# Optimization experiments

Measured on AMD Instinct MI355X. Metric: run time of the kernel, lower is better.

The kernel has to match this reference:

```python
import jax, jax.numpy as jnp
import numpy as np

N = 100_000        # nodes
E = 3_200_000      # edges (avg degree 32)
F_IN = 256         # feature_num
HID = 32           # hard-coded hidden dim in TwoLayerModel
F_OUT = 64         # output_num


def setup_inputs() -> dict:
    key = jax.random.key(0)
    k0, k1, k2, k3 = jax.random.split(key, 4)
    x = jax.random.normal(k0, (N, F_IN), dtype=jnp.float32)
    edge_index = jax.random.randint(k1, (2, E), 0, N, dtype=jnp.int32)
    # glorot-ish init for the two linear weights, zero bias (matches reset_parameters)
    W1 = jax.random.normal(k2, (F_IN, HID), dtype=jnp.float32) * np.float32(1.0 / np.sqrt(F_IN))
    b1 = jnp.zeros((HID,), dtype=jnp.float32)
    W2 = jax.random.normal(k3, (HID, F_OUT), dtype=jnp.float32) * np.float32(1.0 / np.sqrt(HID))
    b2 = jnp.zeros((F_OUT,), dtype=jnp.float32)
    return {"x": x, "edge_index": edge_index, "W1": W1, "b1": b1, "W2": W2, "b2": b2}


def _gcn_propagate(h, row, col, n):
    """Symmetric-normalized sum aggregation: out[i] = sum_{(j->i)} d_j^-1/2 d_i^-1/2 h[j].
    Matches PyG gcn_norm / NewSampleModelLayer edge_weight (deg computed on col)."""
    deg = jax.ops.segment_sum(jnp.ones_like(col, dtype=h.dtype), col, num_segments=n)
    dinv = jnp.where(deg > 0, deg ** -0.5, 0.0)
    norm = dinv[row] * dinv[col]                      # [E']
    return jax.ops.segment_sum(norm[:, None] * h[row], col, num_segments=n)


def reference(x, edge_index, W1, b1, W2, b2):
    n = x.shape[0]
    sl = jnp.arange(n, dtype=edge_index.dtype)
    row = jnp.concatenate([edge_index[0], sl])        # add self-loops
    col = jnp.concatenate([edge_index[1], sl])
    # layer 1: GCNConv(feature_num, 32) -> relu (dropout inactive in eval)
    h = _gcn_propagate(x @ W1, row, col, n) + b1
    h = jax.nn.relu(h)
    # layer 2 (NewSampleModelLayer, eval path): propagate then linear projection
    fr = _gcn_propagate(h, row, col, n)
    return fr @ W2 + b2
```

## Files before the change

### kernel.cpp

```cpp
#include <hip/hip_runtime.h>
#include <hip/hip_fp16.h>
#include <math.h>


#define SHIFT1 8
#define S1 256
#define MAXNB1 400

typedef _Float16 half8 __attribute__((ext_vector_type(8)));
typedef float f32x4 __attribute__((ext_vector_type(4)));

__global__ void k_zero(int* p, int n) {
    int i = blockIdx.x * blockDim.x + threadIdx.x;
    if (i < n) p[i] = 0;
}

__global__ void k_hist1(const int4* __restrict__ cols4, int* __restrict__ bcnt,
                        int e4, int etail, const int* __restrict__ cols, int nb) {
    __shared__ int h[MAXNB1];
    for (int i = threadIdx.x; i < nb; i += blockDim.x) h[i] = 0;
    __syncthreads();
    for (int i = blockIdx.x * blockDim.x + threadIdx.x; i < e4; i += gridDim.x * blockDim.x) {
        int4 c = cols4[i];
        atomicAdd(&h[c.x >> SHIFT1], 1);
        atomicAdd(&h[c.y >> SHIFT1], 1);
        atomicAdd(&h[c.z >> SHIFT1], 1);
        atomicAdd(&h[c.w >> SHIFT1], 1);
    }
    if (blockIdx.x == 0 && threadIdx.x < etail)
        atomicAdd(&h[cols[e4 * 4 + threadIdx.x] >> SHIFT1], 1);
    __syncthreads();
    for (int i = threadIdx.x; i < nb; i += blockDim.x)
        if (h[i]) atomicAdd(&bcnt[i], h[i]);
}

__global__ void k_scan1(const int* __restrict__ bcnt, int* __restrict__ bptr,
                        int* __restrict__ bfill, int nb, int e) {
    __shared__ int sh[512];
    int tid = threadIdx.x;
    int v = (tid < nb) ? bcnt[tid] : 0;
    sh[tid] = v;
    __syncthreads();
    for (int off = 1; off < 512; off <<= 1) {
        int t = (tid >= off) ? sh[tid - off] : 0;
        __syncthreads();
        sh[tid] += t;
        __syncthreads();
    }
    int excl = sh[tid] - v;
    if (tid < nb) { bptr[tid] = excl; bfill[tid] = excl; }
    if (tid == 0) bptr[nb] = e;
}

__launch_bounds__(1024)
__global__ void k_scatter1(const int* __restrict__ rows, const int* __restrict__ cols,
                           int* bfill, unsigned* __restrict__ pk, int e, int nb, int chunk) {
    __shared__ int hist[MAXNB1];
    int tid = threadIdx.x;
    for (int i = tid; i < nb; i += blockDim.x) hist[i] = 0;
    __syncthreads();
    int start = blockIdx.x * chunk;
    int end = min(e, start + chunk);
    for (int i = start + tid; i < end; i += blockDim.x)
        atomicAdd(&hist[cols[i] >> SHIFT1], 1);
    __syncthreads();
    for (int i = tid; i < nb; i += blockDim.x) {
        int c = hist[i];
        if (c) hist[i] = atomicAdd(&bfill[i], c);
    }
    __syncthreads();
    for (int i = start + tid; i < end; i += blockDim.x) {
        int r = rows[i], c = cols[i];
        int pos = atomicAdd(&hist[c >> SHIFT1], 1);
        pk[pos] = ((unsigned)r << SHIFT1) | (unsigned)(c & (S1 - 1));
    }
}

__launch_bounds__(512)
__global__ void k_fine256(const unsigned* __restrict__ pk, const int* __restrict__ bptr,
                          int* __restrict__ erow, int* __restrict__ ptr,
                          float* __restrict__ dinv, int n, int nb) {
    __shared__ int cnt[S1], sh[S1], fill[S1];
    int tid = threadIdx.x, b = blockIdx.x;
    if (tid < S1) cnt[tid] = 0;
    __syncthreads();
    int s = bptr[b], e = bptr[b + 1];
    for (int t = s + tid; t < e; t += 512)
        atomicAdd(&cnt[pk[t] & (S1 - 1)], 1);
    __syncthreads();
    int v = (tid < S1) ? cnt[tid] : 0;
    if (tid < S1) sh[tid] = v;
    __syncthreads();
    for (int off = 1; off < S1; off <<= 1) {
        int t = (tid >= off && tid < S1) ? sh[tid - off] : 0;
        __syncthreads();
        if (tid < S1) sh[tid] += t;
        __syncthreads();
    }
    if (tid < S1) {
        int base = sh[tid] - v;
        fill[tid] = base;
        int node = (b << SHIFT1) + tid;
        if (node < n) {
            ptr[node] = s + base;
            dinv[node] = rsqrtf((float)(v + 1));
        }
    }
    if (b == nb - 1 && tid == 0) ptr[n] = e;
    __syncthreads();
    for (int t = s + tid; t < e; t += 512) {
        unsigned p = pk[t];
        int pos = atomicAdd(&fill[p & (S1 - 1)], 1);
        erow[s + pos] = (int)(p >> SHIFT1);
    }
}

__launch_bounds__(256)
__global__ void k_xw_mfma(const float4* __restrict__ x4, const float4* __restrict__ W1_4,
                          const float* __restrict__ dinv, _Float16* __restrict__ g1h, int n) {
    __shared__ _Float16 xh[64][264];
    __shared__ _Float16 w1t[32][264];
    int tid = threadIdx.x;
    int base = blockIdx.x * 64;
#pragma unroll
    for (int t = 0; t < 16; ++t) {
        int idx = tid + t * 256;
        int row = idx >> 6, c4 = idx & 63;
        float4 v = (base + row < n) ? x4[(size_t)(base + row) * 64 + c4]
                                    : make_float4(0.f, 0.f, 0.f, 0.f);
        __half2 a = __floats2half2_rn(v.x, v.y);
        __half2 b = __floats2half2_rn(v.z, v.w);
        *reinterpret_cast<int2*>(&xh[row][c4 * 4]) = make_int2(*(int*)&a, *(int*)&b);
    }
#pragma unroll
    for (int t = 0; t < 8; ++t) {
        int idx = tid + t * 256;
        int kk = idx >> 3, n4 = idx & 7;
        float4 w = W1_4[idx];
        w1t[n4 * 4 + 0][kk] = (_Float16)w.x;
        w1t[n4 * 4 + 1][kk] = (_Float16)w.y;
        w1t[n4 * 4 + 2][kk] = (_Float16)w.z;
        w1t[n4 * 4 + 3][kk] = (_Float16)w.w;
    }
    __syncthreads();
    int wid = tid >> 6, lane = tid & 63;
    int lrow = lane & 15, kgrp = lane >> 4;
    const _Float16* ap  = &xh[wid * 16 + lrow][kgrp * 8];
    const _Float16* bp0 = &w1t[lrow][kgrp * 8];
    const _Float16* bp1 = &w1t[16 + lrow][kgrp * 8];
    f32x4 acc0 = {0.f, 0.f, 0.f, 0.f}, acc1 = {0.f, 0.f, 0.f, 0.f};
#pragma unroll
    for (int kk = 0; kk < 8; ++kk) {
        half8 a  = *reinterpret_cast<const half8*>(ap + kk * 32);
        half8 b0 = *reinterpret_cast<const half8*>(bp0 + kk * 32);
        half8 b1 = *reinterpret_cast<const half8*>(bp1 + kk * 32);
        acc0 = __builtin_amdgcn_mfma_f32_16x16x32_f16(a, b0, acc0, 0, 0, 0);
        acc1 = __builtin_amdgcn_mfma_f32_16x16x32_f16(a, b1, acc1, 0, 0, 0);
    }
#pragma unroll
    for (int r = 0; r < 4; ++r) {
        int node = base + wid * 16 + kgrp * 4 + r;
        if (node < n) {
            float d = dinv[node];
            g1h[(size_t)node * 32 + lrow]      = (_Float16)(acc0[r] * d);
            g1h[(size_t)node * 32 + 16 + lrow] = (_Float16)(acc1[r] * d);
        }
    }
}

__device__ inline void acc8(float* a, float4 q) {
    const __half2* h = reinterpret_cast<const __half2*>(&q);
#pragma unroll
    for (int i = 0; i < 4; ++i) {
        float2 f = __half22float2(h[i]);
        a[2 * i] += f.x; a[2 * i + 1] += f.y;
    }
}

__launch_bounds__(256)
__global__ void k_agg1(const float4* __restrict__ g1h4, const int* __restrict__ erow,
                       const int* __restrict__ ptr, const float* __restrict__ dinv,
                       const float* __restrict__ b1, int4* __restrict__ g2h4, int n) {
    int tid = threadIdx.x;
    int g = tid >> 2, l = tid & 3;
    int node = blockIdx.x * 64 + g;
    if (node >= n) return;
    int s = ptr[node], e = ptr[node + 1];
    float a[8] = {0, 0, 0, 0, 0, 0, 0, 0};
    float b[8] = {0, 0, 0, 0, 0, 0, 0, 0};
    acc8(a, g1h4[(size_t)node * 4 + l]);
    int t = s;
    for (; t + 7 < e; t += 8) {
        int r0 = erow[t],     r1 = erow[t + 1], r2 = erow[t + 2], r3 = erow[t + 3];
        int r4 = erow[t + 4], r5 = erow[t + 5], r6 = erow[t + 6], r7 = erow[t + 7];
        float4 q0 = g1h4[(size_t)r0 * 4 + l];
        float4 q1 = g1h4[(size_t)r1 * 4 + l];
        float4 q2 = g1h4[(size_t)r2 * 4 + l];
        float4 q3 = g1h4[(size_t)r3 * 4 + l];
        float4 q4 = g1h4[(size_t)r4 * 4 + l];
        float4 q5 = g1h4[(size_t)r5 * 4 + l];
        float4 q6 = g1h4[(size_t)r6 * 4 + l];
        float4 q7 = g1h4[(size_t)r7 * 4 + l];
        acc8(a, q0); acc8(b, q1); acc8(a, q2); acc8(b, q3);
        acc8(a, q4); acc8(b, q5); acc8(a, q6); acc8(b, q7);
    }
    for (; t < e; ++t) acc8(a, g1h4[(size_t)erow[t] * 4 + l]);
    float d = dinv[node];
    float4 bb0 = *reinterpret_cast<const float4*>(&b1[l * 8]);
    float4 bb1 = *reinterpret_cast<const float4*>(&b1[l * 8 + 4]);
    float o[8];
#pragma unroll
    for (int i = 0; i < 8; ++i) {
        float bi = i < 4 ? (&bb0.x)[i] : (&bb1.x)[i - 4];
        float h = fmaf(d, a[i] + b[i], bi);
        o[i] = (h > 0.f ? h : 0.f) * d;
    }
    __half2 h0 = __floats2half2_rn(o[0], o[1]);
    __half2 h1 = __floats2half2_rn(o[2], o[3]);
    __half2 h2 = __floats2half2_rn(o[4], o[5]);
    __half2 h3 = __floats2half2_rn(o[6], o[7]);
    g2h4[(size_t)node * 4 + l] = make_int4(*(int*)&h0, *(int*)&h1, *(int*)&h2, *(int*)&h3);
}

__launch_bounds__(256)
__global__ void k_agg2(const float4* __restrict__ g2h4, const int* __restrict__ erow,
                       const int* __restrict__ ptr, const float* __restrict__ dinv,
                       const float* __restrict__ W2, const float* __restrict__ b2,
                       float* __restrict__ out, int n) {
    __shared__ float fr[64][33];
    __shared__ float w2s[32 * 64];
    int tid = threadIdx.x;
    for (int t = tid; t < 32 * 64; t += 256) w2s[t] = W2[t];
    int g = tid >> 2, l = tid & 3;
    int node = blockIdx.x * 64 + g;
    float a[8] = {0, 0, 0, 0, 0, 0, 0, 0};
    float b[8] = {0, 0, 0, 0, 0, 0, 0, 0};
    float d = 0.f;
    if (node < n) {
        int s = ptr[node], e = ptr[node + 1];
        acc8(a, g2h4[(size_t)node * 4 + l]);
        int t = s;
        for (; t + 7 < e; t += 8) {
            int r0 = erow[t],     r1 = erow[t + 1], r2 = erow[t + 2], r3 = erow[t + 3];
            int r4 = erow[t + 4], r5 = erow[t + 5], r6 = erow[t + 6], r7 = erow[t + 7];
            float4 q0 = g2h4[(size_t)r0 * 4 + l];
            float4 q1 = g2h4[(size_t)r1 * 4 + l];
            float4 q2 = g2h4[(size_t)r2 * 4 + l];
            float4 q3 = g2h4[(size_t)r3 * 4 + l];
            float4 q4 = g2h4[(size_t)r4 * 4 + l];
            float4 q5 = g2h4[(size_t)r5 * 4 + l];
            float4 q6 = g2h4[(size_t)r6 * 4 + l];
            float4 q7 = g2h4[(size_t)r7 * 4 + l];
            acc8(a, q0); acc8(b, q1); acc8(a, q2); acc8(b, q3);
            acc8(a, q4); acc8(b, q5); acc8(a, q6); acc8(b, q7);
        }
        for (; t < e; ++t) acc8(a, g2h4[(size_t)erow[t] * 4 + l]);
        d = dinv[node];
    }
#pragma unroll
    for (int i = 0; i < 8; ++i) fr[g][l * 8 + i] = d * (a[i] + b[i]);
    __syncthreads();
    int j = tid & 63, mg = tid >> 6;
    for (int mm = 0; mm < 16; ++mm) {
        int m = mg * 16 + mm;
        int node2 = blockIdx.x * 64 + m;
        if (node2 >= n) continue;
        float sacc = b2[j];
#pragma unroll
        for (int i = 0; i < 32; ++i)
            sacc = fmaf(fr[m][i], w2s[i * 64 + j], sacc);
        out[(size_t)node2 * 64 + j] = sacc;
    }
}

extern "C" void kernel_launch(void* const* d_in, const int* in_sizes, int n_in,
                              void* d_out, int out_size, void* d_ws, size_t ws_size,
                              hipStream_t stream) {
    const float* x  = (const float*)d_in[0];
    const int*   ei = (const int*)d_in[1];
    const float* W1 = (const float*)d_in[2];
    const float* b1 = (const float*)d_in[3];
    const float* W2 = (const float*)d_in[4];
    const float* b2 = (const float*)d_in[5];
    float* out = (float*)d_out;

    const int N = in_sizes[0] / 256;
    const int E = in_sizes[1] / 2;
    const int* rows = ei;
    const int* cols = ei + E;
    const int NB1 = (N + S1 - 1) >> SHIFT1;

    size_t sz0 = (size_t)E > (size_t)N * 16 ? (size_t)E : (size_t)N * 16;
    unsigned* pk  = (unsigned*)d_ws;
    _Float16* g1h = (_Float16*)d_ws;
    int*      erow = (int*)((char*)d_ws + sz0 * 4);
    _Float16* g2h  = (_Float16*)(erow + E);
    float*    dinv = (float*)((char*)(erow + E) + (size_t)N * 32 * 2);
    int*      ptr  = (int*)(dinv + N);
    int*      bptr1 = ptr + (N + 1);
    int*      bcnt1 = bptr1 + (NB1 + 1);
    int*      bfill1 = bcnt1 + NB1;

    const int B = 256;
    const int e4 = E / 4, etail = E - e4 * 4;
    const int SCB = 256;
    const int chunk = (E + SCB - 1) / SCB;
    const int nblk64 = (N + 63) / 64;

    k_zero<<<(NB1 + B - 1) / B, B, 0, stream>>>(bcnt1, NB1);
    k_hist1<<<256, B, 0, stream>>>((const int4*)cols, bcnt1, e4, etail, cols, NB1);
    k_scan1<<<1, 512, 0, stream>>>(bcnt1, bptr1, bfill1, NB1, E);
    k_scatter1<<<SCB, 1024, 0, stream>>>(rows, cols, bfill1, pk, E, NB1, chunk);
    k_fine256<<<NB1, 512, 0, stream>>>(pk, bptr1, erow, ptr, dinv, N, NB1);
    k_xw_mfma<<<nblk64, B, 0, stream>>>((const float4*)x, (const float4*)W1, dinv, g1h, N);
    k_agg1<<<nblk64, B, 0, stream>>>((const float4*)g1h, erow, ptr, dinv, b1, (int4*)g2h, N);
    k_agg2<<<nblk64, B, 0, stream>>>((const float4*)g2h, erow, ptr, dinv, W2, b2, out, N);
}
```

Measured before the change: 203.8 us.

## Split hidden features into two 16-wide planes to shrink gather working set

```diff
diff --git a/kernel.cpp b/kernel.cpp
--- a/kernel.cpp
+++ b/kernel.cpp
@@ -117,7 +117,8 @@
 
 __launch_bounds__(256)
 __global__ void k_xw_mfma(const float4* __restrict__ x4, const float4* __restrict__ W1_4,
-                          const float* __restrict__ dinv, _Float16* __restrict__ g1h, int n) {
+                          const float* __restrict__ dinv, _Float16* __restrict__ g1lo,
+                          _Float16* __restrict__ g1hi, int n) {
     __shared__ _Float16 xh[64][264];
     __shared__ _Float16 w1t[32][264];
     int tid = threadIdx.x;
@@ -162,8 +163,8 @@
         int node = base + wid * 16 + kgrp * 4 + r;
         if (node < n) {
             float d = dinv[node];
-            g1h[(size_t)node * 32 + lrow]      = (_Float16)(acc0[r] * d);
-            g1h[(size_t)node * 32 + 16 + lrow] = (_Float16)(acc1[r] * d);
+            g1lo[(size_t)node * 16 + lrow] = (_Float16)(acc0[r] * d);
+            g1hi[(size_t)node * 16 + lrow] = (_Float16)(acc1[r] * d);
         }
     }
 }
@@ -177,37 +178,42 @@
     }
 }
 
+#define GATHER_PLANE(gsrc)                                                        \
+    float a[8] = {0, 0, 0, 0, 0, 0, 0, 0};                                        \
+    float b[8] = {0, 0, 0, 0, 0, 0, 0, 0};                                        \
+    {                                                                             \
+        acc8(a, gsrc[(size_t)node * 2 + l]);                                      \
+        int t = s;                                                                \
+        for (; t + 7 < e; t += 8) {                                               \
+            int r0 = erow[t],     r1 = erow[t + 1], r2 = erow[t + 2], r3 = erow[t + 3]; \
+            int r4 = erow[t + 4], r5 = erow[t + 5], r6 = erow[t + 6], r7 = erow[t + 7]; \
+            float4 q0 = gsrc[(size_t)r0 * 2 + l];                                 \
+            float4 q1 = gsrc[(size_t)r1 * 2 + l];                                 \
+            float4 q2 = gsrc[(size_t)r2 * 2 + l];                                 \
+            float4 q3 = gsrc[(size_t)r3 * 2 + l];                                 \
+            float4 q4 = gsrc[(size_t)r4 * 2 + l];                                 \
+            float4 q5 = gsrc[(size_t)r5 * 2 + l];                                 \
+            float4 q6 = gsrc[(size_t)r6 * 2 + l];                                 \
+            float4 q7 = gsrc[(size_t)r7 * 2 + l];                                 \
+            acc8(a, q0); acc8(b, q1); acc8(a, q2); acc8(b, q3);                   \
+            acc8(a, q4); acc8(b, q5); acc8(a, q6); acc8(b, q7);                   \
+        }                                                                         \
+        for (; t < e; ++t) acc8(a, gsrc[(size_t)erow[t] * 2 + l]);                \
+    }
+
 __launch_bounds__(256)
-__global__ void k_agg1(const float4* __restrict__ g1h4, const int* __restrict__ erow,
-                       const int* __restrict__ ptr, const float* __restrict__ dinv,
-                       const float* __restrict__ b1, int4* __restrict__ g2h4, int n) {
-    int tid = threadIdx.x;
-    int g = tid >> 2, l = tid & 3;
-    int node = blockIdx.x * 64 + g;
+__global__ void k_agg1p(const float4* __restrict__ gsrc, const int* __restrict__ erow,
+                        const int* __restrict__ ptr, const float* __restrict__ dinv,
+                        const float* __restrict__ b1f, int4* __restrict__ gdst, int n) {
+    int tid = threadIdx.x;
+    int g = tid >> 1, l = tid & 1;
+    int node = blockIdx.x * 128 + g;
     if (node >= n) return;
     int s = ptr[node], e = ptr[node + 1];
-    float a[8] = {0, 0, 0, 0, 0, 0, 0, 0};
-    float b[8] = {0, 0, 0, 0, 0, 0, 0, 0};
-    acc8(a, g1h4[(size_t)node * 4 + l]);
-    int t = s;
-    for (; t + 7 < e; t += 8) {
-        int r0 = erow[t],     r1 = erow[t + 1], r2 = erow[t + 2], r3 = erow[t + 3];
-        int r4 = erow[t + 4], r5 = erow[t + 5], r6 = erow[t + 6], r7 = erow[t + 7];
-        float4 q0 = g1h4[(size_t)r0 * 4 + l];
-        float4 q1 = g1h4[(size_t)r1 * 4 + l];
-        float4 q2 = g1h4[(size_t)r2 * 4 + l];
-        float4 q3 = g1h4[(size_t)r3 * 4 + l];
-        float4 q4 = g1h4[(size_t)r4 * 4 + l];
-        float4 q5 = g1h4[(size_t)r5 * 4 + l];
-        float4 q6 = g1h4[(size_t)r6 * 4 + l];
-        float4 q7 = g1h4[(size_t)r7 * 4 + l];
-        acc8(a, q0); acc8(b, q1); acc8(a, q2); acc8(b, q3);
-        acc8(a, q4); acc8(b, q5); acc8(a, q6); acc8(b, q7);
-    }
-    for (; t < e; ++t) acc8(a, g1h4[(size_t)erow[t] * 4 + l]);
+    GATHER_PLANE(gsrc)
     float d = dinv[node];
-    float4 bb0 = *reinterpret_cast<const float4*>(&b1[l * 8]);
-    float4 bb1 = *reinterpret_cast<const float4*>(&b1[l * 8 + 4]);
+    float4 bb0 = *reinterpret_cast<const float4*>(&b1f[l * 8]);
+    float4 bb1 = *reinterpret_cast<const float4*>(&b1f[l * 8 + 4]);
     float o[8];
 #pragma unroll
     for (int i = 0; i < 8; ++i) {
@@ -219,51 +225,55 @@
     __half2 h1 = __floats2half2_rn(o[2], o[3]);
     __half2 h2 = __floats2half2_rn(o[4], o[5]);
     __half2 h3 = __floats2half2_rn(o[6], o[7]);
-    g2h4[(size_t)node * 4 + l] = make_int4(*(int*)&h0, *(int*)&h1, *(int*)&h2, *(int*)&h3);
+    gdst[(size_t)node * 2 + l] = make_int4(*(int*)&h0, *(int*)&h1, *(int*)&h2, *(int*)&h3);
 }
 
 __launch_bounds__(256)
-__global__ void k_agg2(const float4* __restrict__ g2h4, const int* __restrict__ erow,
-                       const int* __restrict__ ptr, const float* __restrict__ dinv,
-                       const float* __restrict__ W2, const float* __restrict__ b2,
-                       float* __restrict__ out, int n) {
-    __shared__ float fr[64][33];
+__global__ void k_agg2a(const float4* __restrict__ gsrc, const int* __restrict__ erow,
+                        const int* __restrict__ ptr, const float* __restrict__ dinv,
+                        float* __restrict__ frA, int n) {
+    int tid = threadIdx.x;
+    int g = tid >> 1, l = tid & 1;
+    int node = blockIdx.x * 128 + g;
+    if (node >= n) return;
+    int s = ptr[node], e = ptr[node + 1];
+    GATHER_PLANE(gsrc)
+    float d = dinv[node];
+    float4 o0 = make_float4(d * (a[0] + b[0]), d * (a[1] + b[1]),
+                            d * (a[2] + b[2]), d * (a[3] + b[3]));
+    float4 o1 = make_float4(d * (a[4] + b[4]), d * (a[5] + b[5]),
+                            d * (a[6] + b[6]), d * (a[7] + b[7]));
+    *reinterpret_cast<float4*>(&frA[(size_t)node * 16 + l * 8])     = o0;
+    *reinterpret_cast<float4*>(&frA[(size_t)node * 16 + l * 8 + 4]) = o1;
+}
+
+__launch_bounds__(256)
+__global__ void k_agg2b(const float4* __restrict__ gsrc, const int* __restrict__ erow,
+                        const int* __restrict__ ptr, const float* __restrict__ dinv,
+                        const float4* __restrict__ frA4, const float* __restrict__ W2,
+                        const float* __restrict__ b2, float* __restrict__ out, int n) {
+    __shared__ float fr[128][33];
     __shared__ float w2s[32 * 64];
     int tid = threadIdx.x;
     for (int t = tid; t < 32 * 64; t += 256) w2s[t] = W2[t];
-    int g = tid >> 2, l = tid & 3;
-    int node = blockIdx.x * 64 + g;
-    float a[8] = {0, 0, 0, 0, 0, 0, 0, 0};
-    float b[8] = {0, 0, 0, 0, 0, 0, 0, 0};
-    float d = 0.f;
+    int g = tid >> 1, l = tid & 1;
+    int node = blockIdx.x * 128 + g;
     if (node < n) {
         int s = ptr[node], e = ptr[node + 1];
-        acc8(a, g2h4[(size_t)node * 4 + l]);
-        int t = s;
-        for (; t + 7 < e; t += 8) {
-            int r0 = erow[t],     r1 = erow[t + 1], r2 = erow[t + 2], r3 = erow[t + 3];
-            int r4 = erow[t + 4], r5 = erow[t + 5], r6 = erow[t + 6], r7 = erow[t + 7];
-            float4 q0 = g2h4[(size_t)r0 * 4 + l];
-            float4 q1 = g2h4[(size_t)r1 * 4 + l];
-            float4 q2 = g2h4[(size_t)r2 * 4 + l];
-            float4 q3 = g2h4[(size_t)r3 * 4 + l];
-            float4 q4 = g2h4[(size_t)r4 * 4 + l];
-            float4 q5 = g2h4[(size_t)r5 * 4 + l];
-            float4 q6 = g2h4[(size_t)r6 * 4 + l];
-            float4 q7 = g2h4[(size_t)r7 * 4 + l];
-            acc8(a, q0); acc8(b, q1); acc8(a, q2); acc8(b, q3);
-            acc8(a, q4); acc8(b, q5); acc8(a, q6); acc8(b, q7);
-        }
-        for (; t < e; ++t) acc8(a, g2h4[(size_t)erow[t] * 4 + l]);
-        d = dinv[node];
-    }
-#pragma unroll
-    for (int i = 0; i < 8; ++i) fr[g][l * 8 + i] = d * (a[i] + b[i]);
+        GATHER_PLANE(gsrc)
+        float d = dinv[node];
+        float4 fa = frA4[(size_t)node * 4 + l * 2];
+        float4 fb = frA4[(size_t)node * 4 + l * 2 + 1];
+        *reinterpret_cast<float4*>(&fr[g][l * 8])     = fa;
+        *reinterpret_cast<float4*>(&fr[g][l * 8 + 4]) = fb;
+#pragma unroll
+        for (int i = 0; i < 8; ++i) fr[g][16 + l * 8 + i] = d * (a[i] + b[i]);
+    }
     __syncthreads();
     int j = tid & 63, mg = tid >> 6;
-    for (int mm = 0; mm < 16; ++mm) {
-        int m = mg * 16 + mm;
-        int node2 = blockIdx.x * 64 + m;
+    for (int mm = 0; mm < 32; ++mm) {
+        int m = mg * 32 + mm;
+        int node2 = blockIdx.x * 128 + m;
         if (node2 >= n) continue;
         float sacc = b2[j];
 #pragma unroll
@@ -289,30 +299,39 @@
     const int* rows = ei;
     const int* cols = ei + E;
     const int NB1 = (N + S1 - 1) >> SHIFT1;
-
-    size_t sz0 = (size_t)E > (size_t)N * 16 ? (size_t)E : (size_t)N * 16;
-    unsigned* pk  = (unsigned*)d_ws;
-    _Float16* g1h = (_Float16*)d_ws;
+    const size_t N16 = (size_t)N * 16;
+
+    size_t sz0 = (size_t)E > N16 ? (size_t)E : N16;
+    unsigned* pk   = (unsigned*)d_ws;
+    _Float16* g1p  = (_Float16*)d_ws;
     int*      erow = (int*)((char*)d_ws + sz0 * 4);
-    _Float16* g2h  = (_Float16*)(erow + E);
+    _Float16* g2p  = (_Float16*)(erow + E);
     float*    dinv = (float*)((char*)(erow + E) + (size_t)N * 32 * 2);
     int*      ptr  = (int*)(dinv + N);
     int*      bptr1 = ptr + (N + 1);
     int*      bcnt1 = bptr1 + (NB1 + 1);
     int*      bfill1 = bcnt1 + NB1;
+    float*    frA  = (float*)(bfill1 + NB1);
 
     const int B = 256;
     const int e4 = E / 4, etail = E - e4 * 4;
     const int SCB = 256;
     const int chunk = (E + SCB - 1) / SCB;
     const int nblk64 = (N + 63) / 64;
+    const int nblk128 = (N + 127) / 128;
 
     k_zero<<<(NB1 + B - 1) / B, B, 0, stream>>>(bcnt1, NB1);
     k_hist1<<<256, B, 0, stream>>>((const int4*)cols, bcnt1, e4, etail, cols, NB1);
     k_scan1<<<1, 512, 0, stream>>>(bcnt1, bptr1, bfill1, NB1, E);
     k_scatter1<<<SCB, 1024, 0, stream>>>(rows, cols, bfill1, pk, E, NB1, chunk);
     k_fine256<<<NB1, 512, 0, stream>>>(pk, bptr1, erow, ptr, dinv, N, NB1);
-    k_xw_mfma<<<nblk64, B, 0, stream>>>((const float4*)x, (const float4*)W1, dinv, g1h, N);
-    k_agg1<<<nblk64, B, 0, stream>>>((const float4*)g1h, erow, ptr, dinv, b1, (int4*)g2h, N);
-    k_agg2<<<nblk64, B, 0, stream>>>((const float4*)g2h, erow, ptr, dinv, W2, b2, out, N);
-}
+    k_xw_mfma<<<nblk64, B, 0, stream>>>((const float4*)x, (const float4*)W1, dinv,
+                                        g1p, g1p + N16, N);
+    k_agg1p<<<nblk128, B, 0, stream>>>((const float4*)g1p, erow, ptr, dinv,
+                                       b1, (int4*)g2p, N);
+    k_agg1p<<<nblk128, B, 0, stream>>>((const float4*)(g1p + N16), erow, ptr, dinv,
+                                       b1 + 16, (int4*)(g2p + N16), N);
+    k_agg2a<<<nblk128, B, 0, stream>>>((const float4*)g2p, erow, ptr, dinv, frA, N);
+    k_agg2b<<<nblk128, B, 0, stream>>>((const float4*)(g2p + N16), erow, ptr, dinv,
+                                       (const float4*)frA, W2, b2, out, N);
+}
```

Result: slower. 254.1 us (+24.7%).
